# Kernel optimization log

Hardware: AMD Instinct MI355X
Metric: run time of the kernel (lower is better)

The kernel has to match this reference:

```python
import jax, jax.numpy as jnp
import numpy as np

H = 4   # heads
C = 64  # out_channels per head (256 // 4)


def _gat_layer(x, adjf, Wq, Wk, Wv, b):
    # x: [B,N,F]; adjf: [B,N,N] float mask; W*: [F, H*C]; b: [H*C]
    B, N, _ = x.shape
    q = (x @ Wq).reshape(B, N, H, C)
    k = (x @ Wk).reshape(B, N, H, C)
    v = (x @ Wv).reshape(B, N, H, C)
    alpha = jnp.einsum('bnhf,bmhf->bhnm', q, k) / jnp.sqrt(jnp.asarray(C, x.dtype))
    m = adjf[:, None, :, :]                      # [B,1,N,N] broadcast over heads
    # masked softmax: exp over unmasked entries only, zero elsewhere
    a = jnp.where(m > 0, alpha, -1e30)
    a = a - jnp.max(a, axis=-1, keepdims=True)
    e = jnp.exp(a) * m
    p = e / (jnp.sum(e, axis=-1, keepdims=True) + 1e-16)
    out = jnp.einsum('bhnm,bmhf->bnhf', p, v).reshape(B, N, H * C)
    return out + b


def setup_inputs() -> dict:
    key = jax.random.key(0)
    ks = jax.random.split(key, 12)
    B, N, F = 4, 2048, 256
    HC = H * C
    scale = 1.0 / np.sqrt(F)
    inp = {
        'x': jax.random.normal(ks[0], (B, N, F), dtype=jnp.float32),
        'adj': jax.random.randint(ks[1], (B, N, N), 0, 2, dtype=jnp.int32),
        'Wq1': jax.random.uniform(ks[2], (F, HC), jnp.float32, -scale, scale),
        'Wk1': jax.random.uniform(ks[3], (F, HC), jnp.float32, -scale, scale),
        'Wv1': jax.random.uniform(ks[4], (F, HC), jnp.float32, -scale, scale),
        'b1': jnp.zeros((HC,), jnp.float32),
        'Wq2': jax.random.uniform(ks[5], (F, HC), jnp.float32, -scale, scale),
        'Wk2': jax.random.uniform(ks[6], (F, HC), jnp.float32, -scale, scale),
        'Wv2': jax.random.uniform(ks[7], (F, HC), jnp.float32, -scale, scale),
        'b2': jnp.zeros((HC,), jnp.float32),
    }
    return inp


def reference(x, adj, Wq1, Wk1, Wv1, b1, Wq2, Wk2, Wv2, b2):
    adjf = adj.astype(x.dtype)
    h = _gat_layer(x, adjf, Wq1, Wk1, Wv1, b1)   # hidden conv (add=False)
    h = jax.nn.relu(h)
    out = _gat_layer(h, adjf, Wq2, Wk2, Wv2, b2)  # final layer, final_act=None
    return out
```

## Files before the change

kernel.cpp:

```cpp
#include <hip/hip_runtime.h>
#include <hip/hip_fp16.h>
#include <stdint.h>

#define NNODE 2048

typedef _Float16 half8 __attribute__((ext_vector_type(8)));
typedef __fp16   fp16x2 __attribute__((ext_vector_type(2)));
typedef float    f32x16 __attribute__((ext_vector_type(16)));

__device__ __forceinline__ f32x16 zero16() {
    f32x16 z;
    #pragma unroll
    for (int i = 0; i < 16; ++i) z[i] = 0.f;
    return z;
}

__global__ __launch_bounds__(256) void pack_adj(const int* __restrict__ adj,
                                                unsigned long long* __restrict__ adjp) {
    int gid = blockIdx.x * 256 + threadIdx.x;
    unsigned long long m = __ballot(adj[gid] != 0);
    if ((threadIdx.x & 63) == 0) adjp[gid >> 6] = m;
}

__global__ __launch_bounds__(256) void split_x(const float* __restrict__ x,
                                               __half* __restrict__ xhi,
                                               __half* __restrict__ xlo) {
    size_t gid = (size_t)blockIdx.x * 256 + threadIdx.x;
    float4 v = *reinterpret_cast<const float4*>(x + gid * 4);
    float vv[4] = {v.x, v.y, v.z, v.w};
    union { __half h[4]; uint2 u; } ph, pl;
    #pragma unroll
    for (int j = 0; j < 4; ++j) {
        __half hv = __float2half(vv[j]);
        ph.h[j] = hv;
        pl.h[j] = __float2half(vv[j] - __half2float(hv));
    }
    *reinterpret_cast<uint2*>(xhi + gid * 4) = ph.u;
    *reinterpret_cast<uint2*>(xlo + gid * 4) = pl.u;
}

__global__ __launch_bounds__(256) void split_w(
    const float* __restrict__ W0, const float* __restrict__ W1, const float* __restrict__ W2,
    const float* __restrict__ W3, const float* __restrict__ W4, const float* __restrict__ W5,
    __half* __restrict__ wth, __half* __restrict__ wtl)
{
    __shared__ float T[64][65];
    const int which = blockIdx.y;
    const float* __restrict__ W = (which == 0) ? W0 : (which == 1) ? W1 : (which == 2) ? W2
                                 : (which == 3) ? W3 : (which == 4) ? W4 : W5;
    const int kx = (blockIdx.x & 3) * 64, nx = (blockIdx.x >> 2) * 64;
    const int t = threadIdx.x;
    #pragma unroll
    for (int p = 0; p < 4; ++p) {
        int id = p * 256 + t;
        int r = id >> 4, c4 = (id & 15) * 4;
        float4 v4 = *reinterpret_cast<const float4*>(W + (size_t)(kx + r) * 256 + nx + c4);
        T[r][c4 + 0] = v4.x; T[r][c4 + 1] = v4.y; T[r][c4 + 2] = v4.z; T[r][c4 + 3] = v4.w;
    }
    __syncthreads();
    const int n = t >> 2, kc = (t & 3) * 16;
    union { __half h[16]; uint4 u[2]; } hs, ls;
    #pragma unroll
    for (int i = 0; i < 16; ++i) {
        float v = T[kc + i][n];
        __half hv = __float2half(v);
        hs.h[i] = hv;
        ls.h[i] = __float2half(v - __half2float(hv));
    }
    size_t dst = ((size_t)(which * 256) + nx + n) * 256 + kx + kc;
    *reinterpret_cast<uint4*>(&wth[dst])     = hs.u[0];
    *reinterpret_cast<uint4*>(&wth[dst + 8]) = hs.u[1];
    *reinterpret_cast<uint4*>(&wtl[dst])     = ls.u[0];
    *reinterpret_cast<uint4*>(&wtl[dst + 8]) = ls.u[1];
}

__global__ __launch_bounds__(256) void qkv_gemm_mfma(
    const __half* __restrict__ xh, const __half* __restrict__ xl,
    const __half* __restrict__ wth, const __half* __restrict__ wtl, const int wbase,
    __half* __restrict__ Qhi, __half* __restrict__ Qlo,
    __half* __restrict__ Khi, __half* __restrict__ Klo,
    float* __restrict__ V)
{
    const int row0 = blockIdx.x * 64;
    const int nblk = blockIdx.y;
    const int which = nblk >> 2;
    const int h = nblk & 3;
    const int tid = threadIdx.x;
    const int wave = tid >> 6, lane = tid & 63;
    const int lq = lane & 31, hh = lane >> 5;
    const int wm = wave >> 1, wn = wave & 1;

    const size_t woff = ((size_t)((wbase + which) * 256) + h * 64 + wn * 32 + lq) * 256 + 8 * hh;
    const __half* __restrict__ wt_h = wth + woff;
    const __half* __restrict__ wt_l = wtl + woff;
    const size_t xoff = (size_t)(row0 + 32 * wm + lq) * 256 + 8 * hh;
    const __half* __restrict__ xr_h = xh + xoff;
    const __half* __restrict__ xr_l = xl + xoff;

    f32x16 st = zero16();
    #pragma unroll 4
    for (int ks = 0; ks < 16; ++ks) {
        half8 ah = *reinterpret_cast<const half8*>(xr_h + ks * 16);
        half8 al = *reinterpret_cast<const half8*>(xr_l + ks * 16);
        half8 bh = *reinterpret_cast<const half8*>(wt_h + ks * 16);
        half8 bl = *reinterpret_cast<const half8*>(wt_l + ks * 16);
        st = __builtin_amdgcn_mfma_f32_32x32x16_f16(ah, bh, st, 0, 0, 0);
        st = __builtin_amdgcn_mfma_f32_32x32x16_f16(al, bh, st, 0, 0, 0);
        st = __builtin_amdgcn_mfma_f32_32x32x16_f16(ah, bl, st, 0, 0, 0);
    }

    const int c = wn * 32 + lq;
    if (which == 2) {
        #pragma unroll
        for (int r = 0; r < 16; ++r) {
            int row = row0 + 32 * wm + (r & 3) + 8 * (r >> 2) + 4 * hh;
            int b = row >> 11, n = row & 2047;
            V[((size_t)(b * 4 + h) * 2048 + n) * 64 + c] = st[r];
        }
    } else if (which == 0) {
        #pragma unroll
        for (int r = 0; r < 16; ++r) {
            int row = row0 + 32 * wm + (r & 3) + 8 * (r >> 2) + 4 * hh;
            int b = row >> 11, n = row & 2047;
            size_t idx = ((size_t)(b * 4 + h) * 2048 + n) * 64 + c;
            float v = st[r] * 0.125f;
            __half hv = __float2half(v);
            Qhi[idx] = hv;
            Qlo[idx] = __float2half(v - __half2float(hv));
        }
    } else {
        #pragma unroll
        for (int r = 0; r < 16; ++r) {
            int row = row0 + 32 * wm + (r & 3) + 8 * (r >> 2) + 4 * hh;
            int b = row >> 11, n = row & 2047;
            size_t idx = (((size_t)(b * 4 + h) * 64 + (n >> 5)) * 4 + (c >> 4)) * 512
                         + (size_t)(n & 31) * 16 + (c & 15);
            float v = st[r];
            __half hv = __float2half(v);
            Khi[idx] = hv;
            Klo[idx] = __float2half(v - __half2float(hv));
        }
    }
}

__global__ __launch_bounds__(256) void transpose_split_v(
    const float* __restrict__ V, __half* __restrict__ vthi, __half* __restrict__ vtlo)
{
    __shared__ float T[64][65];
    const int bh = blockIdx.y;
    const int m0 = blockIdx.x * 64;
    const float* __restrict__ Vb = V + (size_t)bh * 2048 * 64;
    const int t = threadIdx.x;
    #pragma unroll
    for (int p = 0; p < 4; ++p) {
        int id = p * 256 + t;
        int m = id >> 4;
        int c4 = (id & 15) * 4;
        float4 v4 = *reinterpret_cast<const float4*>(Vb + (size_t)(m0 + m) * 64 + c4);
        T[m][c4 + 0] = v4.x; T[m][c4 + 1] = v4.y; T[m][c4 + 2] = v4.z; T[m][c4 + 3] = v4.w;
    }
    __syncthreads();
    const int c = t >> 2, g = t & 3;
    union { __half h[16]; uint4 u[2]; } hs, ls;
    #pragma unroll
    for (int i = 0; i < 16; ++i) {
        float v = T[g * 16 + i][c];
        __half hv = __float2half(v);
        hs.h[i] = hv;
        ls.h[i] = __float2half(v - __half2float(hv));
    }
    size_t dst = (((size_t)bh * 128) + (m0 >> 4) + g) * 1024 + (size_t)c * 16;
    *reinterpret_cast<uint4*>(&vthi[dst])     = hs.u[0];
    *reinterpret_cast<uint4*>(&vthi[dst + 8]) = hs.u[1];
    *reinterpret_cast<uint4*>(&vtlo[dst])     = ls.u[0];
    *reinterpret_cast<uint4*>(&vtlo[dst + 8]) = ls.u[1];
}

__global__ __launch_bounds__(256) void gat_attn(
    const __half* __restrict__ qhi, const __half* __restrict__ qlo,
    const __half* __restrict__ khi, const __half* __restrict__ klo,
    const __half* __restrict__ vthi, const __half* __restrict__ vtlo,
    const unsigned long long* __restrict__ adjp,
    const float* __restrict__ bias, float* __restrict__ out,
    __half* __restrict__ hhi, __half* __restrict__ hlo, const int mode)
{
    const int lid = (blockIdx.x & 7) * 128 + (blockIdx.x >> 3);
    const int bh = lid >> 6, qt = lid & 63;
    const int b = bh >> 2, h = bh & 3;
    const int tid = threadIdx.x;
    const int wave = tid >> 6;
    const int lane = tid & 63;
    const int lq = lane & 31;
    const int hh = lane >> 5;
    const int q0 = qt * 32;

    const size_t qkbase = (size_t)bh * 2048 * 64;

    half8 qfh[4], qfl[4];
    {
        const __half* qr_h = qhi + qkbase + (size_t)(q0 + lq) * 64 + 8 * hh;
        const __half* qr_l = qlo + qkbase + (size_t)(q0 + lq) * 64 + 8 * hh;
        #pragma unroll
        for (int ks = 0; ks < 4; ++ks) {
            qfh[ks] = *reinterpret_cast<const half8*>(qr_h + ks * 16);
            qfl[ks] = *reinterpret_cast<const half8*>(qr_l + ks * 16);
        }
    }

    f32x16 o0 = zero16(), o1 = zero16();
    float mrun = -1e30f, lrun = 0.f;

    const unsigned long long* __restrict__ wrow = adjp + (size_t)(b * 2048 + q0 + lq) * 32;
    const int mbase = wave * 512;

    #pragma unroll 1
    for (int mw = 0; mw < 512; mw += 64) {
        const int mglob = mbase + mw;
        const unsigned long long wmask = wrow[mglob >> 6];

        #pragma unroll
        for (int hi2 = 0; hi2 < 2; ++hi2) {
            const int mt = mglob + hi2 * 32;

            const __half* kb_h = khi + ((size_t)(bh * 64) + (mt >> 5)) * 2048 + lq * 16 + 8 * hh;
            const __half* kb_l = klo + ((size_t)(bh * 64) + (mt >> 5)) * 2048 + lq * 16 + 8 * hh;
            f32x16 st = zero16();
            __builtin_amdgcn_s_setprio(1);
            #pragma unroll
            for (int ks = 0; ks < 4; ++ks) {
                half8 kh = *reinterpret_cast<const half8*>(kb_h + ks * 512);
                half8 kl = *reinterpret_cast<const half8*>(kb_l + ks * 512);
                st = __builtin_amdgcn_mfma_f32_32x32x16_f16(kh, qfh[ks], st, 0, 0, 0);
                st = __builtin_amdgcn_mfma_f32_32x32x16_f16(kl, qfh[ks], st, 0, 0, 0);
                st = __builtin_amdgcn_mfma_f32_32x32x16_f16(kh, qfl[ks], st, 0, 0, 0);
            }
            __builtin_amdgcn_s_setprio(0);

            const __half* vb_h = vthi + ((size_t)(bh * 128) + (mt >> 4)) * 1024 + lq * 16 + 8 * hh;
            const __half* vb_l = vtlo + ((size_t)(bh * 128) + (mt >> 4)) * 1024 + lq * 16 + 8 * hh;
            half8 va0h = *reinterpret_cast<const half8*>(vb_h);
            half8 vb0h = *reinterpret_cast<const half8*>(vb_h + 512);
            half8 va0l = *reinterpret_cast<const half8*>(vb_l);
            half8 vb0l = *reinterpret_cast<const half8*>(vb_l + 512);

            const unsigned int v32 = (unsigned int)(wmask >> (hi2 * 32));
            const unsigned int w2 = v32 >> (4 * hh);
            const unsigned int bits = (w2 & 0xFu) | ((w2 >> 4) & 0xF0u)
                                    | ((w2 >> 8) & 0xF00u) | ((w2 >> 12) & 0xF000u);
            float tv[16];
            float pm = -1e30f;
            #pragma unroll
            for (int i = 0; i < 16; ++i) {
                tv[i] = ((bits >> i) & 1u) ? st[i] : -1e30f;
                pm = fmaxf(pm, tv[i]);
            }
            pm = fmaxf(pm, __shfl_xor(pm, 32, 64));
            if (!__all(pm <= mrun)) {
                float mnew = fmaxf(mrun, pm);
                float sf = __expf(mrun - mnew);
                mrun = mnew;
                lrun *= sf;
                o0 *= sf;
                o1 *= sf;
            }
            float e[16];
            #pragma unroll
            for (int i = 0; i < 16; ++i)
                e[i] = ((bits >> i) & 1u) ? __expf(tv[i] - mrun) : 0.f;
            float ps = (((e[0] + e[1]) + (e[2] + e[3])) + ((e[4] + e[5]) + (e[6] + e[7])))
                     + (((e[8] + e[9]) + (e[10] + e[11])) + ((e[12] + e[13]) + (e[14] + e[15])));
            ps += __shfl_xor(ps, 32, 64);
            lrun += ps;

            half8 va1h, vb1h, va1l, vb1l;
            #pragma unroll
            for (int t2 = 0; t2 < 2; ++t2) {
                unsigned int Hp[4], Lp[4];
                #pragma unroll
                for (int p2 = 0; p2 < 4; ++p2) {
                    float ea = e[8 * t2 + 2 * p2], eb = e[8 * t2 + 2 * p2 + 1];
                    union { fp16x2 f; unsigned int u; } ch, cl;
                    ch.f = __builtin_amdgcn_cvt_pkrtz(ea, eb);
                    float fa = (float)ch.f[0], fb = (float)ch.f[1];
                    cl.f = __builtin_amdgcn_cvt_pkrtz(ea - fa, eb - fb);
                    Hp[p2] = ch.u; Lp[p2] = cl.u;
                }
                unsigned int hr1 = (unsigned)__shfl_xor((int)(hh ? Hp[0] : Hp[2]), 32, 64);
                unsigned int hr2 = (unsigned)__shfl_xor((int)(hh ? Hp[1] : Hp[3]), 32, 64);
                unsigned int lr1 = (unsigned)__shfl_xor((int)(hh ? Lp[0] : Lp[2]), 32, 64);
                unsigned int lr2 = (unsigned)__shfl_xor((int)(hh ? Lp[1] : Lp[3]), 32, 64);
                union { unsigned int u[4]; half8 hv; } Bh, Bl;
                Bh.u[0] = hh ? hr1 : Hp[0]; Bh.u[1] = hh ? hr2 : Hp[1];
                Bh.u[2] = hh ? Hp[2] : hr1; Bh.u[3] = hh ? Hp[3] : hr2;
                Bl.u[0] = hh ? lr1 : Lp[0]; Bl.u[1] = hh ? lr2 : Lp[1];
                Bl.u[2] = hh ? Lp[2] : lr1; Bl.u[3] = hh ? Lp[3] : lr2;

                if (t2 == 0) {
                    va1h = *reinterpret_cast<const half8*>(vb_h + 1024);
                    vb1h = *reinterpret_cast<const half8*>(vb_h + 1536);
                    va1l = *reinterpret_cast<const half8*>(vb_l + 1024);
                    vb1l = *reinterpret_cast<const half8*>(vb_l + 1536);
                }
                half8 vah = t2 ? va1h : va0h;
                half8 val = t2 ? va1l : va0l;
                half8 vbh2 = t2 ? vb1h : vb0h;
                half8 vbl2 = t2 ? vb1l : vb0l;

                __builtin_amdgcn_s_setprio(1);
                o0 = __builtin_amdgcn_mfma_f32_32x32x16_f16(vah, Bh.hv, o0, 0, 0, 0);
                o0 = __builtin_amdgcn_mfma_f32_32x32x16_f16(val, Bh.hv, o0, 0, 0, 0);
                o0 = __builtin_amdgcn_mfma_f32_32x32x16_f16(vah, Bl.hv, o0, 0, 0, 0);
                o1 = __builtin_amdgcn_mfma_f32_32x32x16_f16(vbh2, Bh.hv, o1, 0, 0, 0);
                o1 = __builtin_amdgcn_mfma_f32_32x32x16_f16(vbl2, Bh.hv, o1, 0, 0, 0);
                o1 = __builtin_amdgcn_mfma_f32_32x32x16_f16(vbh2, Bl.hv, o1, 0, 0, 0);
                __builtin_amdgcn_s_setprio(0);
            }
        }
    }

    __shared__ float OS[4][64][33];
    __shared__ float MS[4][32];
    __shared__ float LS[4][32];

    #pragma unroll
    for (int ct = 0; ct < 2; ++ct) {
        #pragma unroll
        for (int i = 0; i < 16; ++i) {
            int c = 32 * ct + (i & 3) + 8 * (i >> 2) + 4 * hh;
            OS[wave][c][lq] = ct ? o1[i] : o0[i];
        }
    }
    if (hh == 0) { MS[wave][lq] = mrun; LS[wave][lq] = lrun; }
    __syncthreads();

    const int q = tid >> 3, c8 = (tid & 7) * 8;
    float m0v = MS[0][q], m1v = MS[1][q], m2v = MS[2][q], m3v = MS[3][q];
    float M = fmaxf(fmaxf(m0v, m1v), fmaxf(m2v, m3v));
    float w0 = __expf(m0v - M), w1 = __expf(m1v - M), w2w = __expf(m2v - M), w3 = __expf(m3v - M);
    float L = LS[0][q] * w0 + LS[1][q] * w1 + LS[2][q] * w2w + LS[3][q] * w3;
    float inv = 1.f / (L + 1e-16f);
    float res[8];
    #pragma unroll
    for (int j = 0; j < 8; ++j) {
        int c = c8 + j;
        float o = OS[0][c][q] * w0 + OS[1][c][q] * w1 + OS[2][c][q] * w2w + OS[3][c][q] * w3;
        res[j] = o * inv + bias[h * 64 + c];
    }
    size_t oidx = ((size_t)(b * 2048) + q0 + q) * 256 + h * 64 + c8;
    if (mode == 0) {
        union { __half h[8]; uint4 u; } sh, sl;
        #pragma unroll
        for (int j = 0; j < 8; ++j) {
            float val = fmaxf(res[j], 0.f);
            __half hv = __float2half(val);
            sh.h[j] = hv;
            sl.h[j] = __float2half(val - __half2float(hv));
        }
        *reinterpret_cast<uint4*>(&hhi[oidx]) = sh.u;
        *reinterpret_cast<uint4*>(&hlo[oidx]) = sl.u;
    } else {
        *reinterpret_cast<float4*>(&out[oidx])     = make_float4(res[0], res[1], res[2], res[3]);
        *reinterpret_cast<float4*>(&out[oidx + 4]) = make_float4(res[4], res[5], res[6], res[7]);
    }
}

extern "C" void kernel_launch(void* const* d_in, const int* in_sizes, int n_in,
                              void* d_out, int out_size, void* d_ws, size_t ws_size,
                              hipStream_t stream) {
    const float* x   = (const float*)d_in[0];
    const int*   adj = (const int*)d_in[1];
    const float* Wq1 = (const float*)d_in[2];
    const float* Wk1 = (const float*)d_in[3];
    const float* Wv1 = (const float*)d_in[4];
    const float* b1  = (const float*)d_in[5];
    const float* Wq2 = (const float*)d_in[6];
    const float* Wk2 = (const float*)d_in[7];
    const float* Wv2 = (const float*)d_in[8];
    const float* b2  = (const float*)d_in[9];
    float* outp = (float*)d_out;

    char* ws = (char*)d_ws;
    unsigned long long* adjp = (unsigned long long*)ws;
    __half* xhi = (__half*)(ws + ( 2u << 20));
    __half* xlo = (__half*)(ws + ( 6u << 20));
    __half* wth = (__half*)(ws + (10u << 20));
    __half* wtl = (__half*)(ws + (11u << 20));
    __half* qhi = (__half*)(ws + (12u << 20));
    __half* qlo = (__half*)(ws + (16u << 20));
    __half* khi = (__half*)(ws + (20u << 20));
    __half* klo = (__half*)(ws + (24u << 20));
    float*  v   = (float*) (ws + (28u << 20));
    __half* vthi= (__half*)(ws + (36u << 20));
    __half* vtlo= (__half*)(ws + (40u << 20));

    pack_adj<<<65536, 256, 0, stream>>>(adj, adjp);
    split_x<<<2048, 256, 0, stream>>>(x, xhi, xlo);
    split_w<<<dim3(16, 6), 256, 0, stream>>>(Wq1, Wk1, Wv1, Wq2, Wk2, Wv2, wth, wtl);

    qkv_gemm_mfma<<<dim3(128, 12), 256, 0, stream>>>(xhi, xlo, wth, wtl, 0,
                                                     qhi, qlo, khi, klo, v);
    transpose_split_v<<<dim3(32, 16), 256, 0, stream>>>(v, vthi, vtlo);
    gat_attn<<<1024, 256, 0, stream>>>(qhi, qlo, khi, klo, vthi, vtlo, adjp, b1,
                                       outp, xhi, xlo, 0);

    qkv_gemm_mfma<<<dim3(128, 12), 256, 0, stream>>>(xhi, xlo, wth, wtl, 3,
                                                     qhi, qlo, khi, klo, v);
    transpose_split_v<<<dim3(32, 16), 256, 0, stream>>>(v, vthi, vtlo);
    gat_attn<<<1024, 256, 0, stream>>>(qhi, qlo, khi, klo, vthi, vtlo, adjp, b2,
                                       outp, xhi, xlo, 1);
}
```

Baseline: 379.5 us.

## Fuse V transpose-split into QKV GEMM and prefetch K tiles in attention

```diff
diff --git a/kernel.cpp b/kernel.cpp
--- a/kernel.cpp
+++ b/kernel.cpp
@@ -79,7 +79,7 @@
     const __half* __restrict__ wth, const __half* __restrict__ wtl, const int wbase,
     __half* __restrict__ Qhi, __half* __restrict__ Qlo,
     __half* __restrict__ Khi, __half* __restrict__ Klo,
-    float* __restrict__ V)
+    __half* __restrict__ vthi, __half* __restrict__ vtlo)
 {
     const int row0 = blockIdx.x * 64;
     const int nblk = blockIdx.y;
@@ -112,10 +112,21 @@
     const int c = wn * 32 + lq;
     if (which == 2) {
         #pragma unroll
-        for (int r = 0; r < 16; ++r) {
-            int row = row0 + 32 * wm + (r & 3) + 8 * (r >> 2) + 4 * hh;
-            int b = row >> 11, n = row & 2047;
-            V[((size_t)(b * 4 + h) * 2048 + n) * 64 + c] = st[r];
+        for (int i = 0; i < 4; ++i) {
+            int rowb = row0 + 32 * wm + 8 * i + 4 * hh;
+            int b = rowb >> 11, n = rowb & 2047;
+            size_t dst = (((size_t)(b * 4 + h) * 128) + (n >> 4)) * 1024
+                         + (size_t)c * 16 + (n & 15);
+            union { __half h[4]; uint2 u; } ph, pl;
+            #pragma unroll
+            for (int j = 0; j < 4; ++j) {
+                float v = st[4 * i + j];
+                __half hv = __float2half(v);
+                ph.h[j] = hv;
+                pl.h[j] = __float2half(v - __half2float(hv));
+            }
+            *reinterpret_cast<uint2*>(&vthi[dst]) = ph.u;
+            *reinterpret_cast<uint2*>(&vtlo[dst]) = pl.u;
         }
     } else if (which == 0) {
         #pragma unroll
@@ -143,40 +154,7 @@
     }
 }
 
-__global__ __launch_bounds__(256) void transpose_split_v(
-    const float* __restrict__ V, __half* __restrict__ vthi, __half* __restrict__ vtlo)
-{
-    __shared__ float T[64][65];
-    const int bh = blockIdx.y;
-    const int m0 = blockIdx.x * 64;
-    const float* __restrict__ Vb = V + (size_t)bh * 2048 * 64;
-    const int t = threadIdx.x;
-    #pragma unroll
-    for (int p = 0; p < 4; ++p) {
-        int id = p * 256 + t;
-        int m = id >> 4;
-        int c4 = (id & 15) * 4;
-        float4 v4 = *reinterpret_cast<const float4*>(Vb + (size_t)(m0 + m) * 64 + c4);
-        T[m][c4 + 0] = v4.x; T[m][c4 + 1] = v4.y; T[m][c4 + 2] = v4.z; T[m][c4 + 3] = v4.w;
-    }
-    __syncthreads();
-    const int c = t >> 2, g = t & 3;
-    union { __half h[16]; uint4 u[2]; } hs, ls;
-    #pragma unroll
-    for (int i = 0; i < 16; ++i) {
-        float v = T[g * 16 + i][c];
-        __half hv = __float2half(v);
-        hs.h[i] = hv;
-        ls.h[i] = __float2half(v - __half2float(hv));
-    }
-    size_t dst = (((size_t)bh * 128) + (m0 >> 4) + g) * 1024 + (size_t)c * 16;
-    *reinterpret_cast<uint4*>(&vthi[dst])     = hs.u[0];
-    *reinterpret_cast<uint4*>(&vthi[dst + 8]) = hs.u[1];
-    *reinterpret_cast<uint4*>(&vtlo[dst])     = ls.u[0];
-    *reinterpret_cast<uint4*>(&vtlo[dst + 8]) = ls.u[1];
-}
-
-__global__ __launch_bounds__(256) void gat_attn(
+__global__ __launch_bounds__(256, 4) void gat_attn(
     const __half* __restrict__ qhi, const __half* __restrict__ qlo,
     const __half* __restrict__ khi, const __half* __restrict__ klo,
     const __half* __restrict__ vthi, const __half* __restrict__ vtlo,
@@ -212,110 +190,135 @@
 
     const unsigned long long* __restrict__ wrow = adjp + (size_t)(b * 2048 + q0 + lq) * 32;
     const int mbase = wave * 512;
+    const int klane = lq * 16 + 8 * hh;
+
+    half8 kA[4], kB[4];
+    {
+        const __half* kp = khi + ((size_t)(bh * 64) + (mbase >> 5)) * 2048 + klane;
+        #pragma unroll
+        for (int ks = 0; ks < 4; ++ks) kA[ks] = *reinterpret_cast<const half8*>(kp + ks * 512);
+    }
+
+    unsigned long long wm64 = 0;
+
+    auto tile_body = [&](half8 (&khc)[4], half8 (&khn)[4], int tt) {
+        const int mt = mbase + 32 * tt;
+
+        if ((tt & 1) == 0) wm64 = wrow[mt >> 6];
+        const unsigned int v32 = (unsigned int)(wm64 >> ((tt & 1) * 32));
+
+        const __half* klp = klo + ((size_t)(bh * 64) + (mt >> 5)) * 2048 + klane;
+        half8 klv[4];
+        #pragma unroll
+        for (int ks = 0; ks < 4; ++ks) klv[ks] = *reinterpret_cast<const half8*>(klp + ks * 512);
+
+        f32x16 st = zero16();
+        __builtin_amdgcn_s_setprio(1);
+        #pragma unroll
+        for (int ks = 0; ks < 4; ++ks)
+            st = __builtin_amdgcn_mfma_f32_32x32x16_f16(khc[ks], qfh[ks], st, 0, 0, 0);
+        #pragma unroll
+        for (int ks = 0; ks < 4; ++ks)
+            st = __builtin_amdgcn_mfma_f32_32x32x16_f16(khc[ks], qfl[ks], st, 0, 0, 0);
+        #pragma unroll
+        for (int ks = 0; ks < 4; ++ks)
+            st = __builtin_amdgcn_mfma_f32_32x32x16_f16(klv[ks], qfh[ks], st, 0, 0, 0);
+        __builtin_amdgcn_s_setprio(0);
+
+        {
+            const int mtn = (tt < 15) ? mt + 32 : mbase;
+            const __half* knp = khi + ((size_t)(bh * 64) + (mtn >> 5)) * 2048 + klane;
+            #pragma unroll
+            for (int ks = 0; ks < 4; ++ks) khn[ks] = *reinterpret_cast<const half8*>(knp + ks * 512);
+        }
+
+        const __half* vb_h = vthi + ((size_t)(bh * 128) + (mt >> 4)) * 1024 + klane;
+        const __half* vb_l = vtlo + ((size_t)(bh * 128) + (mt >> 4)) * 1024 + klane;
+        half8 va0h = *reinterpret_cast<const half8*>(vb_h);
+        half8 vb0h = *reinterpret_cast<const half8*>(vb_h + 512);
+        half8 va0l = *reinterpret_cast<const half8*>(vb_l);
+        half8 vb0l = *reinterpret_cast<const half8*>(vb_l + 512);
+
+        const unsigned int w2 = v32 >> (4 * hh);
+        const unsigned int bits = (w2 & 0xFu) | ((w2 >> 4) & 0xF0u)
+                                | ((w2 >> 8) & 0xF00u) | ((w2 >> 12) & 0xF000u);
+        float tv[16];
+        #pragma unroll
+        for (int i = 0; i < 16; ++i)
+            tv[i] = ((bits >> i) & 1u) ? st[i] : -1e30f;
+        float a0 = fmaxf(fmaxf(tv[0], tv[1]), tv[2]);
+        float a1 = fmaxf(fmaxf(tv[3], tv[4]), tv[5]);
+        float a2 = fmaxf(fmaxf(tv[6], tv[7]), tv[8]);
+        float a3 = fmaxf(fmaxf(tv[9], tv[10]), tv[11]);
+        float a4 = fmaxf(fmaxf(tv[12], tv[13]), tv[14]);
+        float pm = fmaxf(fmaxf(fmaxf(a0, a1), fmaxf(a2, a3)), fmaxf(a4, tv[15]));
+        pm = fmaxf(pm, __shfl_xor(pm, 32, 64));
+        if (!__all(pm <= mrun)) {
+            float mnew = fmaxf(mrun, pm);
+            float sf = __expf(mrun - mnew);
+            mrun = mnew;
+            lrun *= sf;
+            o0 *= sf;
+            o1 *= sf;
+        }
+        float e[16];
+        #pragma unroll
+        for (int i = 0; i < 16; ++i)
+            e[i] = ((bits >> i) & 1u) ? __expf(tv[i] - mrun) : 0.f;
+        float ps = (((e[0] + e[1]) + (e[2] + e[3])) + ((e[4] + e[5]) + (e[6] + e[7])))
+                 + (((e[8] + e[9]) + (e[10] + e[11])) + ((e[12] + e[13]) + (e[14] + e[15])));
+        ps += __shfl_xor(ps, 32, 64);
+        lrun += ps;
+
+        half8 va1h, vb1h, va1l, vb1l;
+        #pragma unroll
+        for (int t2 = 0; t2 < 2; ++t2) {
+            unsigned int Hp[4], Lp[4];
+            #pragma unroll
+            for (int p2 = 0; p2 < 4; ++p2) {
+                float ea = e[8 * t2 + 2 * p2], eb = e[8 * t2 + 2 * p2 + 1];
+                union { fp16x2 f; unsigned int u; } ch, cl;
+                ch.f = __builtin_amdgcn_cvt_pkrtz(ea, eb);
+                float fa = (float)ch.f[0], fb = (float)ch.f[1];
+                cl.f = __builtin_amdgcn_cvt_pkrtz(ea - fa, eb - fb);
+                Hp[p2] = ch.u; Lp[p2] = cl.u;
+            }
+            unsigned int hr1 = (unsigned)__shfl_xor((int)(hh ? Hp[0] : Hp[2]), 32, 64);
+            unsigned int hr2 = (unsigned)__shfl_xor((int)(hh ? Hp[1] : Hp[3]), 32, 64);
+            unsigned int lr1 = (unsigned)__shfl_xor((int)(hh ? Lp[0] : Lp[2]), 32, 64);
+            unsigned int lr2 = (unsigned)__shfl_xor((int)(hh ? Lp[1] : Lp[3]), 32, 64);
+            union { unsigned int u[4]; half8 hv; } Bh, Bl;
+            Bh.u[0] = hh ? hr1 : Hp[0]; Bh.u[1] = hh ? hr2 : Hp[1];
+            Bh.u[2] = hh ? Hp[2] : hr1; Bh.u[3] = hh ? Hp[3] : hr2;
+            Bl.u[0] = hh ? lr1 : Lp[0]; Bl.u[1] = hh ? lr2 : Lp[1];
+            Bl.u[2] = hh ? Lp[2] : lr1; Bl.u[3] = hh ? Lp[3] : lr2;
+
+            if (t2 == 0) {
+                va1h = *reinterpret_cast<const half8*>(vb_h + 1024);
+                vb1h = *reinterpret_cast<const half8*>(vb_h + 1536);
+                va1l = *reinterpret_cast<const half8*>(vb_l + 1024);
+                vb1l = *reinterpret_cast<const half8*>(vb_l + 1536);
+            }
+            half8 vah  = t2 ? va1h : va0h;
+            half8 val  = t2 ? va1l : va0l;
+            half8 vbh2 = t2 ? vb1h : vb0h;
+            half8 vbl2 = t2 ? vb1l : vb0l;
+
+            __builtin_amdgcn_s_setprio(1);
+            o0 = __builtin_amdgcn_mfma_f32_32x32x16_f16(vah, Bh.hv, o0, 0, 0, 0);
+            o0 = __builtin_amdgcn_mfma_f32_32x32x16_f16(val, Bh.hv, o0, 0, 0, 0);
+            o0 = __builtin_amdgcn_mfma_f32_32x32x16_f16(vah, Bl.hv, o0, 0, 0, 0);
+            o1 = __builtin_amdgcn_mfma_f32_32x32x16_f16(vbh2, Bh.hv, o1, 0, 0, 0);
+            o1 = __builtin_amdgcn_mfma_f32_32x32x16_f16(vbl2, Bh.hv, o1, 0, 0, 0);
+            o1 = __builtin_amdgcn_mfma_f32_32x32x16_f16(vbh2, Bl.hv, o1, 0, 0, 0);
+            __builtin_amdgcn_s_setprio(0);
+        }
+    };
 
     #pragma unroll 1
-    for (int mw = 0; mw < 512; mw += 64) {
-        const int mglob = mbase + mw;
-        const unsigned long long wmask = wrow[mglob >> 6];
-
-        #pragma unroll
-        for (int hi2 = 0; hi2 < 2; ++hi2) {
-            const int mt = mglob + hi2 * 32;
-
-            const __half* kb_h = khi + ((size_t)(bh * 64) + (mt >> 5)) * 2048 + lq * 16 + 8 * hh;
-            const __half* kb_l = klo + ((size_t)(bh * 64) + (mt >> 5)) * 2048 + lq * 16 + 8 * hh;
-            f32x16 st = zero16();
-            __builtin_amdgcn_s_setprio(1);
-            #pragma unroll
-            for (int ks = 0; ks < 4; ++ks) {
-                half8 kh = *reinterpret_cast<const half8*>(kb_h + ks * 512);
-                half8 kl = *reinterpret_cast<const half8*>(kb_l + ks * 512);
-                st = __builtin_amdgcn_mfma_f32_32x32x16_f16(kh, qfh[ks], st, 0, 0, 0);
-                st = __builtin_amdgcn_mfma_f32_32x32x16_f16(kl, qfh[ks], st, 0, 0, 0);
-                st = __builtin_amdgcn_mfma_f32_32x32x16_f16(kh, qfl[ks], st, 0, 0, 0);
-            }
-            __builtin_amdgcn_s_setprio(0);
-
-            const __half* vb_h = vthi + ((size_t)(bh * 128) + (mt >> 4)) * 1024 + lq * 16 + 8 * hh;
-            const __half* vb_l = vtlo + ((size_t)(bh * 128) + (mt >> 4)) * 1024 + lq * 16 + 8 * hh;
-            half8 va0h = *reinterpret_cast<const half8*>(vb_h);
-            half8 vb0h = *reinterpret_cast<const half8*>(vb_h + 512);
-            half8 va0l = *reinterpret_cast<const half8*>(vb_l);
-            half8 vb0l = *reinterpret_cast<const half8*>(vb_l + 512);
-
-            const unsigned int v32 = (unsigned int)(wmask >> (hi2 * 32));
-            const unsigned int w2 = v32 >> (4 * hh);
-            const unsigned int bits = (w2 & 0xFu) | ((w2 >> 4) & 0xF0u)
-                                    | ((w2 >> 8) & 0xF00u) | ((w2 >> 12) & 0xF000u);
-            float tv[16];
-            float pm = -1e30f;
-            #pragma unroll
-            for (int i = 0; i < 16; ++i) {
-                tv[i] = ((bits >> i) & 1u) ? st[i] : -1e30f;
-                pm = fmaxf(pm, tv[i]);
-            }
-            pm = fmaxf(pm, __shfl_xor(pm, 32, 64));
-            if (!__all(pm <= mrun)) {
-                float mnew = fmaxf(mrun, pm);
-                float sf = __expf(mrun - mnew);
-                mrun = mnew;
-                lrun *= sf;
-                o0 *= sf;
-                o1 *= sf;
-            }
-            float e[16];
-            #pragma unroll
-            for (int i = 0; i < 16; ++i)
-                e[i] = ((bits >> i) & 1u) ? __expf(tv[i] - mrun) : 0.f;
-            float ps = (((e[0] + e[1]) + (e[2] + e[3])) + ((e[4] + e[5]) + (e[6] + e[7])))
-                     + (((e[8] + e[9]) + (e[10] + e[11])) + ((e[12] + e[13]) + (e[14] + e[15])));
-            ps += __shfl_xor(ps, 32, 64);
-            lrun += ps;
-
-            half8 va1h, vb1h, va1l, vb1l;
-            #pragma unroll
-            for (int t2 = 0; t2 < 2; ++t2) {
-                unsigned int Hp[4], Lp[4];
-                #pragma unroll
-                for (int p2 = 0; p2 < 4; ++p2) {
-                    float ea = e[8 * t2 + 2 * p2], eb = e[8 * t2 + 2 * p2 + 1];
-                    union { fp16x2 f; unsigned int u; } ch, cl;
-                    ch.f = __builtin_amdgcn_cvt_pkrtz(ea, eb);
-                    float fa = (float)ch.f[0], fb = (float)ch.f[1];
-                    cl.f = __builtin_amdgcn_cvt_pkrtz(ea - fa, eb - fb);
-                    Hp[p2] = ch.u; Lp[p2] = cl.u;
-                }
-                unsigned int hr1 = (unsigned)__shfl_xor((int)(hh ? Hp[0] : Hp[2]), 32, 64);
-                unsigned int hr2 = (unsigned)__shfl_xor((int)(hh ? Hp[1] : Hp[3]), 32, 64);
-                unsigned int lr1 = (unsigned)__shfl_xor((int)(hh ? Lp[0] : Lp[2]), 32, 64);
-                unsigned int lr2 = (unsigned)__shfl_xor((int)(hh ? Lp[1] : Lp[3]), 32, 64);
-                union { unsigned int u[4]; half8 hv; } Bh, Bl;
-                Bh.u[0] = hh ? hr1 : Hp[0]; Bh.u[1] = hh ? hr2 : Hp[1];
-                Bh.u[2] = hh ? Hp[2] : hr1; Bh.u[3] = hh ? Hp[3] : hr2;
-                Bl.u[0] = hh ? lr1 : Lp[0]; Bl.u[1] = hh ? lr2 : Lp[1];
-                Bl.u[2] = hh ? Lp[2] : lr1; Bl.u[3] = hh ? Lp[3] : lr2;
-
-                if (t2 == 0) {
-                    va1h = *reinterpret_cast<const half8*>(vb_h + 1024);
-                    vb1h = *reinterpret_cast<const half8*>(vb_h + 1536);
-                    va1l = *reinterpret_cast<const half8*>(vb_l + 1024);
-                    vb1l = *reinterpret_cast<const half8*>(vb_l + 1536);
-                }
-                half8 vah = t2 ? va1h : va0h;
-                half8 val = t2 ? va1l : va0l;
-                half8 vbh2 = t2 ? vb1h : vb0h;
-                half8 vbl2 = t2 ? vb1l : vb0l;
-
-                __builtin_amdgcn_s_setprio(1);
-                o0 = __builtin_amdgcn_mfma_f32_32x32x16_f16(vah, Bh.hv, o0, 0, 0, 0);
-                o0 = __builtin_amdgcn_mfma_f32_32x32x16_f16(val, Bh.hv, o0, 0, 0, 0);
-                o0 = __builtin_amdgcn_mfma_f32_32x32x16_f16(vah, Bl.hv, o0, 0, 0, 0);
-                o1 = __builtin_amdgcn_mfma_f32_32x32x16_f16(vbh2, Bh.hv, o1, 0, 0, 0);
-                o1 = __builtin_amdgcn_mfma_f32_32x32x16_f16(vbl2, Bh.hv, o1, 0, 0, 0);
-                o1 = __builtin_amdgcn_mfma_f32_32x32x16_f16(vbh2, Bl.hv, o1, 0, 0, 0);
-                __builtin_amdgcn_s_setprio(0);
-            }
-        }
+    for (int tt2 = 0; tt2 < 8; ++tt2) {
+        tile_body(kA, kB, 2 * tt2);
+        tile_body(kB, kA, 2 * tt2 + 1);
     }
 
     __shared__ float OS[4][64][33];
@@ -389,7 +392,6 @@
     __half* qlo = (__half*)(ws + (16u << 20));
     __half* khi = (__half*)(ws + (20u << 20));
     __half* klo = (__half*)(ws + (24u << 20));
-    float*  v   = (float*) (ws + (28u << 20));
     __half* vthi= (__half*)(ws + (36u << 20));
     __half* vtlo= (__half*)(ws + (40u << 20));
 
@@ -398,14 +400,12 @@
     split_w<<<dim3(16, 6), 256, 0, stream>>>(Wq1, Wk1, Wv1, Wq2, Wk2, Wv2, wth, wtl);
 
     qkv_gemm_mfma<<<dim3(128, 12), 256, 0, stream>>>(xhi, xlo, wth, wtl, 0,
-                                                     qhi, qlo, khi, klo, v);
-    transpose_split_v<<<dim3(32, 16), 256, 0, stream>>>(v, vthi, vtlo);
+                                                     qhi, qlo, khi, klo, vthi, vtlo);
     gat_attn<<<1024, 256, 0, stream>>>(qhi, qlo, khi, klo, vthi, vtlo, adjp, b1,
                                        outp, xhi, xlo, 0);
 
     qkv_gemm_mfma<<<dim3(128, 12), 256, 0, stream>>>(xhi, xlo, wth, wtl, 3,
-                                                     qhi, qlo, khi, klo, v);
-    transpose_split_v<<<dim3(32, 16), 256, 0, stream>>>(v, vthi, vtlo);
+                                                     qhi, qlo, khi, klo, vthi, vtlo);
     gat_attn<<<1024, 256, 0, stream>>>(qhi, qlo, khi, klo, vthi, vtlo, adjp, b2,
                                        outp, xhi, xlo, 1);
 }
```

Measured after the change: 411.3 us. +8.4%, slower.
